# Kernel tuning notes

Hardware: AMD Instinct MI355X
Metric: run time of the kernel (lower is better)

The kernel has to match this reference:

```python
import jax, jax.numpy as jnp
import numpy as np

N = 50000      # points
K = 16         # neighbors per point
DIM = 256      # channels
H = 8          # heads
HD = DIM // H  # head dim


def setup_inputs() -> dict:
    key = jax.random.key(0)
    ks = jax.random.split(key, 8)
    feats = jax.random.normal(ks[0], (N, DIM), jnp.float32)
    xyz = jax.random.normal(ks[1], (N, 3), jnp.float32)
    # sorted segment ids: each point attends to exactly K neighbors
    index_0 = jnp.repeat(jnp.arange(N, dtype=jnp.int32), K)            # [M]
    index_1 = jax.random.randint(ks[2], (N * K,), 0, N, dtype=jnp.int32)  # [M]
    index_0_offsets = jnp.arange(N + 1, dtype=jnp.int32) * K
    s = 1.0 / np.sqrt(DIM)
    qkv_w = jax.random.normal(ks[3], (3 * DIM, DIM), jnp.float32) * s
    qkv_b = jax.random.normal(ks[4], (3 * DIM,), jnp.float32) * 0.01
    proj_w = jax.random.normal(ks[5], (DIM, DIM), jnp.float32) * s
    proj_b = jax.random.normal(ks[6], (DIM,), jnp.float32) * 0.01
    return {
        'feats': feats, 'xyz': xyz,
        'index_0': index_0, 'index_1': index_1,
        'index_0_offsets': index_0_offsets, 'n_max': K,
        'qkv_w': qkv_w, 'qkv_b': qkv_b, 'proj_w': proj_w, 'proj_b': proj_b,
    }


def reference(feats, xyz, index_0, index_1, index_0_offsets, n_max,
              qkv_w, qkv_b, proj_w, proj_b):
    n, c = feats.shape
    scale = (c // H) ** (-0.5)
    qkv = (feats @ qkv_w.T + qkv_b).reshape(n, 3, H, HD)  # [N,3,H,HD]
    q = qkv[:, 0] * scale
    k = qkv[:, 1]
    v = qkv[:, 2]
    # attention_step1: per-pair gathered dot product -> [M, H]
    attn = jnp.einsum('mhd,mhd->mh', q[index_0], k[index_1])
    # scatter_softmax over segments of index_0 (numerically stable)
    seg_max = jax.ops.segment_max(attn, index_0, num_segments=n)  # [N,H]
    e = jnp.exp(attn - seg_max[index_0])
    denom = jax.ops.segment_sum(e, index_0, num_segments=n)       # [N,H]
    attn = e / denom[index_0]                                     # [M,H]
    # attention_step2: scatter weighted sum of gathered values -> [N,H,HD]
    x = jax.ops.segment_sum(attn[:, :, None] * v[index_1], index_0,
                            num_segments=n)
    x = x.reshape(n, c)
    return x @ proj_w.T + proj_b
```

## Files before the change

kernel.cpp:

```cpp
#include <hip/hip_runtime.h>
#include <hip/hip_bf16.h>
#include <stdint.h>

typedef __bf16 bf16x8_t __attribute__((ext_vector_type(8)));
typedef float f32x4_t __attribute__((ext_vector_type(4)));

__device__ __forceinline__ float b2f(unsigned short u) {
    union { uint32_t i; float f; } x; x.i = ((uint32_t)u) << 16; return x.f;
}
__device__ __forceinline__ unsigned short f2b(float f) {
    union { float f; uint32_t i; } x; x.f = f;
    uint32_t r = (x.i + 0x7fffu + ((x.i >> 16) & 1u)) >> 16;
    return (unsigned short)r;
}

#define QSCALE 0.17677669529663687f

__global__ void cvt_f32_bf16(const float* __restrict__ in, unsigned short* __restrict__ out, int n) {
    int i = (blockIdx.x * blockDim.x + threadIdx.x) * 4;
    if (i >= n) return;
    const float4 v = *reinterpret_cast<const float4*>(in + i);
    ushort4 o;
    o.x = f2b(v.x); o.y = f2b(v.y); o.z = f2b(v.z); o.w = f2b(v.w);
    *reinterpret_cast<ushort4*>(out + i) = o;
}

__global__ void prep_weights(const float* __restrict__ qkv_w, const float* __restrict__ proj_w,
                             const float* __restrict__ qkv_b,
                             unsigned short* __restrict__ qkvwb, unsigned short* __restrict__ projwb,
                             float* __restrict__ qkvbS) {
    const int idx = blockIdx.x * 256 + threadIdx.x;
    if (idx < 49152) {
        const int e = idx * 4;
        const float4 v = *reinterpret_cast<const float4*>(qkv_w + e);
        const float sc = (e >> 8) < 256 ? QSCALE : 1.f;
        ushort4 o;
        o.x = f2b(v.x * sc); o.y = f2b(v.y * sc); o.z = f2b(v.z * sc); o.w = f2b(v.w * sc);
        *reinterpret_cast<ushort4*>(qkvwb + e) = o;
    } else if (idx < 49152 + 16384) {
        const int e = (idx - 49152) * 4;
        const float4 v = *reinterpret_cast<const float4*>(proj_w + e);
        ushort4 o;
        o.x = f2b(v.x); o.y = f2b(v.y); o.z = f2b(v.z); o.w = f2b(v.w);
        *reinterpret_cast<ushort4*>(projwb + e) = o;
    } else if (idx < 49152 + 16384 + 192) {
        const int e = (idx - 49152 - 16384) * 4;
        float4 v = *reinterpret_cast<const float4*>(qkv_b + e);
        if (e < 256) { v.x *= QSCALE; v.y *= QSCALE; v.z *= QSCALE; v.w *= QSCALE; }
        *reinterpret_cast<float4*>(qkvbS + e) = v;
    }
}

template <int OUT_MODE>
__launch_bounds__(256, 2)
__global__ void gemm_bf16(const unsigned short* __restrict__ A,
                          const unsigned short* __restrict__ W,
                          const float* __restrict__ bias,
                          void* __restrict__ Cout,
                          int M, int Nn, int Kk) {
    const int nCol = Nn >> 7;
    const int p = blockIdx.x;
    const int xcd = p & 7;
    const int q = p >> 3;
    const int c = q % nCol;
    const int rr = q / nCol;
    const int r = rr * 8 + xcd;
    const int blockRow = r * 128;
    if (blockRow >= M) return;
    const int blockCol = c * 128;

    __shared__ unsigned short As[128 * 64];
    __shared__ unsigned short Bs[128 * 64];
    const int t = threadIdx.x;
    const int w = t >> 6;
    const int l = t & 63;
    const int wm = w >> 1, wn = w & 1;

    f32x4_t acc[4][4];
#pragma unroll
    for (int i = 0; i < 4; ++i)
#pragma unroll
        for (int j = 0; j < 4; ++j) acc[i][j] = (f32x4_t)0.f;

    const int srow = t >> 3;
    const int scol = (((t & 7) ^ ((t >> 3) & 7)) * 8);

    for (int k0 = 0; k0 < Kk; k0 += 64) {
#pragma unroll
        for (int cc = 0; cc < 4; ++cc) {
            int arow = blockRow + cc * 32 + srow;
            arow = arow < M ? arow : M - 1;
            const unsigned short* ga = A + (size_t)arow * Kk + k0 + scol;
            const int brow = blockCol + cc * 32 + srow;
            const unsigned short* gb = W + (size_t)brow * Kk + k0 + scol;
            unsigned short* la = &As[cc * 2048 + w * 512];
            unsigned short* lb = &Bs[cc * 2048 + w * 512];
            __builtin_amdgcn_global_load_lds((const __attribute__((address_space(1))) void*)ga,
                                             (__attribute__((address_space(3))) void*)la, 16, 0, 0);
            __builtin_amdgcn_global_load_lds((const __attribute__((address_space(1))) void*)gb,
                                             (__attribute__((address_space(3))) void*)lb, 16, 0, 0);
        }
        __syncthreads();
        const int l15 = l & 15;
        const int lk = l >> 4;
        const int key = l & 7;
#pragma unroll
        for (int kc = 0; kc < 2; ++kc) {
            bf16x8_t af[4], bfr[4];
            const int cb = kc * 4 + lk;
            const int kof = (cb ^ key) * 8;
#pragma unroll
            for (int i = 0; i < 4; ++i) {
                af[i]  = *reinterpret_cast<const bf16x8_t*>(&As[(wm * 64 + i * 16 + l15) * 64 + kof]);
                bfr[i] = *reinterpret_cast<const bf16x8_t*>(&Bs[(wn * 64 + i * 16 + l15) * 64 + kof]);
            }
#pragma unroll
            for (int i = 0; i < 4; ++i)
#pragma unroll
                for (int j = 0; j < 4; ++j)
                    acc[i][j] = __builtin_amdgcn_mfma_f32_16x16x32_bf16(af[i], bfr[j], acc[i][j], 0, 0, 0);
        }
        __syncthreads();
    }

    const int lr = (l >> 4) * 4;
    const int lc = l & 15;
#pragma unroll
    for (int i = 0; i < 4; ++i) {
#pragma unroll
        for (int j = 0; j < 4; ++j) {
            const int col = blockCol + wn * 64 + j * 16 + lc;
            const float bz = bias[col];
#pragma unroll
            for (int rg = 0; rg < 4; ++rg) {
                const int row = blockRow + wm * 64 + i * 16 + lr + rg;
                if (row < M) {
                    const float val = acc[i][j][rg] + bz;
                    if (OUT_MODE == 0) {
                        ((float*)Cout)[(size_t)row * Nn + col] = val;
                    } else {
                        const size_t sec = (size_t)(col >> 8) * (size_t)M * 256;
                        ((unsigned short*)Cout)[sec + (size_t)row * 256 + (col & 255)] = f2b(val);
                    }
                }
            }
        }
    }
}

__global__ void attn_logits(const unsigned short* __restrict__ qb,
                            const unsigned short* __restrict__ kb,
                            const int* __restrict__ index_1,
                            unsigned short* __restrict__ wbuf) {
    const int w = threadIdx.x >> 6;
    const int i = blockIdx.x * 4 + w;
    const int l = threadIdx.x & 63;
    const int h = l >> 3;
    const int p = l & 7;
    const int d0 = p * 4;

    int nbr[16];
#pragma unroll
    for (int m = 0; m < 16; ++m) nbr[m] = index_1[i * 16 + m];

    ushort4 kreg[16];
#pragma unroll
    for (int m = 0; m < 16; ++m)
        kreg[m] = *reinterpret_cast<const ushort4*>(&kb[(size_t)nbr[m] * 256 + h * 32 + d0]);

    const ushort4 qu = *reinterpret_cast<const ushort4*>(&qb[(size_t)i * 256 + h * 32 + d0]);
    const float qx = b2f(qu.x), qy = b2f(qu.y), qz = b2f(qu.z), qw = b2f(qu.w);

    float s[16];
#pragma unroll
    for (int m = 0; m < 16; ++m) {
        float pv = qx * b2f(kreg[m].x) + qy * b2f(kreg[m].y)
                 + qz * b2f(kreg[m].z) + qw * b2f(kreg[m].w);
        pv += __shfl_xor(pv, 1, 8);
        pv += __shfl_xor(pv, 2, 8);
        pv += __shfl_xor(pv, 4, 8);
        s[m] = pv;
    }
    float mx = -1e30f;
#pragma unroll
    for (int m = 0; m < 16; ++m) mx = fmaxf(mx, s[m]);
    float sum = 0.f;
#pragma unroll
    for (int m = 0; m < 16; ++m) { s[m] = __expf(s[m] - mx); sum += s[m]; }
    const float inv = 1.f / sum;

    const uint32_t pack = (uint32_t)f2b(s[2 * p] * inv) | ((uint32_t)f2b(s[2 * p + 1] * inv) << 16);
    ((uint32_t*)wbuf)[(size_t)i * 64 + h * 8 + p] = pack;
}

__global__ void attn_out(const unsigned short* __restrict__ vb,
                         const unsigned short* __restrict__ wbuf,
                         const int* __restrict__ index_1,
                         unsigned short* __restrict__ xb) {
    const int w = threadIdx.x >> 6;
    const int i = blockIdx.x * 4 + w;
    const int l = threadIdx.x & 63;
    const int h = l >> 3;
    const int p = l & 7;
    const int d0 = p * 4;

    int nbr[16];
#pragma unroll
    for (int m = 0; m < 16; ++m) nbr[m] = index_1[i * 16 + m];

    ushort4 vreg[16];
#pragma unroll
    for (int m = 0; m < 16; ++m)
        vreg[m] = *reinterpret_cast<const ushort4*>(&vb[(size_t)nbr[m] * 256 + h * 32 + d0]);

    const uint32_t wp = ((const uint32_t*)wbuf)[(size_t)i * 64 + h * 8 + p];

    float ax = 0.f, ay = 0.f, az = 0.f, aw = 0.f;
#pragma unroll
    for (int m = 0; m < 16; ++m) {
        const uint32_t src = __shfl(wp, h * 8 + (m >> 1), 64);
        const float wt = b2f((unsigned short)((m & 1) ? (src >> 16) : (src & 0xffff)));
        ax += wt * b2f(vreg[m].x); ay += wt * b2f(vreg[m].y);
        az += wt * b2f(vreg[m].z); aw += wt * b2f(vreg[m].w);
    }
    ushort4 o;
    o.x = f2b(ax); o.y = f2b(ay); o.z = f2b(az); o.w = f2b(aw);
    *reinterpret_cast<ushort4*>(&xb[(size_t)i * 256 + h * 32 + d0]) = o;
}

extern "C" void kernel_launch(void* const* d_in, const int* in_sizes, int n_in,
                              void* d_out, int out_size, void* d_ws, size_t ws_size,
                              hipStream_t stream) {
    const float* feats   = (const float*)d_in[0];
    const int*   index_1 = (const int*)d_in[3];
    const float* qkv_w   = (const float*)d_in[6];
    const float* qkv_b   = (const float*)d_in[7];
    const float* proj_w  = (const float*)d_in[8];
    const float* proj_b  = (const float*)d_in[9];
    float* out = (float*)d_out;

    const int N = 50000, DIM = 256, QKVD = 768;

    unsigned short* featsb = (unsigned short*)d_ws;
    unsigned short* qkvwb  = featsb + (size_t)N * DIM;
    unsigned short* projwb = qkvwb + (size_t)QKVD * DIM;
    float*          qkvbS  = (float*)(projwb + (size_t)DIM * DIM);
    unsigned short* qb     = (unsigned short*)(qkvbS + QKVD);
    unsigned short* kb     = qb + (size_t)N * DIM;
    unsigned short* vb     = kb + (size_t)N * DIM;
    unsigned short* xb     = vb + (size_t)N * DIM;
    unsigned short* wbuf   = xb + (size_t)N * DIM;

    cvt_f32_bf16<<<(N * DIM / 4 + 255) / 256, 256, 0, stream>>>(feats, featsb, N * DIM);
    prep_weights<<<(49152 + 16384 + 192 + 255) / 256, 256, 0, stream>>>(
        qkv_w, proj_w, qkv_b, qkvwb, projwb, qkvbS);

    const int nRow = (N + 127) / 128;
    const int nRowPad = ((nRow + 7) / 8) * 8;

    gemm_bf16<1><<<nRowPad * (QKVD / 128), 256, 0, stream>>>(featsb, qkvwb, qkvbS, qb, N, QKVD, DIM);
    attn_logits<<<N / 4, 256, 0, stream>>>(qb, kb, index_1, wbuf);
    attn_out<<<N / 4, 256, 0, stream>>>(vb, wbuf, index_1, xb);
    gemm_bf16<0><<<nRowPad * (DIM / 128), 256, 0, stream>>>(xb, projwb, proj_b, out, N, DIM, DIM);
}
```

Baseline: 294.4 us.

## Remap attention kernels to one thread per point-head and merge prep kernels

The logits and aggregation kernels now give each thread a whole head (32 dims) of one point, with 8 points per wavefront. Each thread issues 16-byte loads and does the dot products serially, which removes the cross-lane shuffle reductions and the weight broadcast shuffles. The weight buffer layout changes to per-head contiguous 16 weights. The feature conversion and weight prep kernels are merged into one launch. The cost is much higher register use per thread (32 accumulators plus 64 bytes per neighbour load), which may lower occupancy, and less coalesced access across lanes.

```diff
diff --git a/kernel.cpp b/kernel.cpp
--- a/kernel.cpp
+++ b/kernel.cpp
@@ -13,38 +13,42 @@
     uint32_t r = (x.i + 0x7fffu + ((x.i >> 16) & 1u)) >> 16;
     return (unsigned short)r;
 }
+__device__ __forceinline__ void up2(uint32_t d, float& lo, float& hi) {
+    union { uint32_t u; float f; } a, b;
+    a.u = d << 16; b.u = d & 0xffff0000u;
+    lo = a.f; hi = b.f;
+}
 
 #define QSCALE 0.17677669529663687f
-
-__global__ void cvt_f32_bf16(const float* __restrict__ in, unsigned short* __restrict__ out, int n) {
-    int i = (blockIdx.x * blockDim.x + threadIdx.x) * 4;
-    if (i >= n) return;
-    const float4 v = *reinterpret_cast<const float4*>(in + i);
-    ushort4 o;
-    o.x = f2b(v.x); o.y = f2b(v.y); o.z = f2b(v.z); o.w = f2b(v.w);
-    *reinterpret_cast<ushort4*>(out + i) = o;
-}
-
-__global__ void prep_weights(const float* __restrict__ qkv_w, const float* __restrict__ proj_w,
-                             const float* __restrict__ qkv_b,
-                             unsigned short* __restrict__ qkvwb, unsigned short* __restrict__ projwb,
-                             float* __restrict__ qkvbS) {
+#define NQ 50000
+
+__global__ void prep_all(const float* __restrict__ feats, const float* __restrict__ qkv_w,
+                         const float* __restrict__ proj_w, const float* __restrict__ qkv_b,
+                         unsigned short* __restrict__ featsb, unsigned short* __restrict__ qkvwb,
+                         unsigned short* __restrict__ projwb, float* __restrict__ qkvbS) {
     const int idx = blockIdx.x * 256 + threadIdx.x;
-    if (idx < 49152) {
+    const int NF = NQ * 256 / 4;
+    if (idx < NF) {
         const int e = idx * 4;
+        const float4 v = *reinterpret_cast<const float4*>(feats + e);
+        ushort4 o;
+        o.x = f2b(v.x); o.y = f2b(v.y); o.z = f2b(v.z); o.w = f2b(v.w);
+        *reinterpret_cast<ushort4*>(featsb + e) = o;
+    } else if (idx < NF + 49152) {
+        const int e = (idx - NF) * 4;
         const float4 v = *reinterpret_cast<const float4*>(qkv_w + e);
         const float sc = (e >> 8) < 256 ? QSCALE : 1.f;
         ushort4 o;
         o.x = f2b(v.x * sc); o.y = f2b(v.y * sc); o.z = f2b(v.z * sc); o.w = f2b(v.w * sc);
         *reinterpret_cast<ushort4*>(qkvwb + e) = o;
-    } else if (idx < 49152 + 16384) {
-        const int e = (idx - 49152) * 4;
+    } else if (idx < NF + 49152 + 16384) {
+        const int e = (idx - NF - 49152) * 4;
         const float4 v = *reinterpret_cast<const float4*>(proj_w + e);
         ushort4 o;
         o.x = f2b(v.x); o.y = f2b(v.y); o.z = f2b(v.z); o.w = f2b(v.w);
         *reinterpret_cast<ushort4*>(projwb + e) = o;
-    } else if (idx < 49152 + 16384 + 192) {
-        const int e = (idx - 49152 - 16384) * 4;
+    } else if (idx < NF + 49152 + 16384 + 192) {
+        const int e = (idx - NF - 49152 - 16384) * 4;
         float4 v = *reinterpret_cast<const float4*>(qkv_b + e);
         if (e < 256) { v.x *= QSCALE; v.y *= QSCALE; v.z *= QSCALE; v.w *= QSCALE; }
         *reinterpret_cast<float4*>(qkvbS + e) = v;
@@ -148,84 +152,118 @@
     }
 }
 
-__global__ void attn_logits(const unsigned short* __restrict__ qb,
-                            const unsigned short* __restrict__ kb,
-                            const int* __restrict__ index_1,
-                            unsigned short* __restrict__ wbuf) {
+__global__ void attn_logits2(const unsigned short* __restrict__ qb,
+                             const unsigned short* __restrict__ kb,
+                             const int* __restrict__ index_1,
+                             unsigned short* __restrict__ wbuf) {
     const int w = threadIdx.x >> 6;
-    const int i = blockIdx.x * 4 + w;
     const int l = threadIdx.x & 63;
-    const int h = l >> 3;
-    const int p = l & 7;
-    const int d0 = p * 4;
-
-    int nbr[16];
-#pragma unroll
-    for (int m = 0; m < 16; ++m) nbr[m] = index_1[i * 16 + m];
-
-    ushort4 kreg[16];
-#pragma unroll
-    for (int m = 0; m < 16; ++m)
-        kreg[m] = *reinterpret_cast<const ushort4*>(&kb[(size_t)nbr[m] * 256 + h * 32 + d0]);
-
-    const ushort4 qu = *reinterpret_cast<const ushort4*>(&qb[(size_t)i * 256 + h * 32 + d0]);
-    const float qx = b2f(qu.x), qy = b2f(qu.y), qz = b2f(qu.z), qw = b2f(qu.w);
+    const int g = l >> 3;
+    const int h = l & 7;
+    int i = blockIdx.x * 32 + w * 8 + g;
+    const bool valid = i < NQ;
+    if (!valid) i = 0;
+
+    const int4* ip = reinterpret_cast<const int4*>(index_1 + (size_t)i * 16);
+    const int4 n0 = ip[0], n1 = ip[1], n2 = ip[2], n3 = ip[3];
+    const int nbr[16] = { n0.x, n0.y, n0.z, n0.w, n1.x, n1.y, n1.z, n1.w,
+                          n2.x, n2.y, n2.z, n2.w, n3.x, n3.y, n3.z, n3.w };
+
+    const uint4* qp = reinterpret_cast<const uint4*>(qb + (size_t)i * 256 + h * 32);
+    const uint4 q0 = qp[0], q1 = qp[1], q2 = qp[2], q3 = qp[3];
+    const uint32_t qd[16] = { q0.x, q0.y, q0.z, q0.w, q1.x, q1.y, q1.z, q1.w,
+                              q2.x, q2.y, q2.z, q2.w, q3.x, q3.y, q3.z, q3.w };
+    float qf[32];
+#pragma unroll
+    for (int j = 0; j < 16; ++j) up2(qd[j], qf[2 * j], qf[2 * j + 1]);
 
     float s[16];
 #pragma unroll
     for (int m = 0; m < 16; ++m) {
-        float pv = qx * b2f(kreg[m].x) + qy * b2f(kreg[m].y)
-                 + qz * b2f(kreg[m].z) + qw * b2f(kreg[m].w);
-        pv += __shfl_xor(pv, 1, 8);
-        pv += __shfl_xor(pv, 2, 8);
-        pv += __shfl_xor(pv, 4, 8);
-        s[m] = pv;
-    }
-    float mx = -1e30f;
-#pragma unroll
-    for (int m = 0; m < 16; ++m) mx = fmaxf(mx, s[m]);
+        const uint4* kp = reinterpret_cast<const uint4*>(kb + (size_t)nbr[m] * 256 + h * 32);
+        const uint4 k0 = kp[0], k1 = kp[1], k2 = kp[2], k3 = kp[3];
+        const uint32_t kd[16] = { k0.x, k0.y, k0.z, k0.w, k1.x, k1.y, k1.z, k1.w,
+                                  k2.x, k2.y, k2.z, k2.w, k3.x, k3.y, k3.z, k3.w };
+        float acc = 0.f;
+#pragma unroll
+        for (int j = 0; j < 16; ++j) {
+            float lo, hi; up2(kd[j], lo, hi);
+            acc += qf[2 * j] * lo;
+            acc += qf[2 * j + 1] * hi;
+        }
+        s[m] = acc;
+    }
+    float mx = s[0];
+#pragma unroll
+    for (int m = 1; m < 16; ++m) mx = fmaxf(mx, s[m]);
     float sum = 0.f;
 #pragma unroll
     for (int m = 0; m < 16; ++m) { s[m] = __expf(s[m] - mx); sum += s[m]; }
     const float inv = 1.f / sum;
 
-    const uint32_t pack = (uint32_t)f2b(s[2 * p] * inv) | ((uint32_t)f2b(s[2 * p + 1] * inv) << 16);
-    ((uint32_t*)wbuf)[(size_t)i * 64 + h * 8 + p] = pack;
-}
-
-__global__ void attn_out(const unsigned short* __restrict__ vb,
-                         const unsigned short* __restrict__ wbuf,
-                         const int* __restrict__ index_1,
-                         unsigned short* __restrict__ xb) {
+    if (valid) {
+        uint32_t o[8];
+#pragma unroll
+        for (int m = 0; m < 8; ++m)
+            o[m] = (uint32_t)f2b(s[2 * m] * inv) | ((uint32_t)f2b(s[2 * m + 1] * inv) << 16);
+        uint4* op = reinterpret_cast<uint4*>(wbuf + (size_t)i * 128 + h * 16);
+        op[0] = make_uint4(o[0], o[1], o[2], o[3]);
+        op[1] = make_uint4(o[4], o[5], o[6], o[7]);
+    }
+}
+
+__global__ void attn_out2(const unsigned short* __restrict__ vb,
+                          const unsigned short* __restrict__ wbuf,
+                          const int* __restrict__ index_1,
+                          unsigned short* __restrict__ xb) {
     const int w = threadIdx.x >> 6;
-    const int i = blockIdx.x * 4 + w;
     const int l = threadIdx.x & 63;
-    const int h = l >> 3;
-    const int p = l & 7;
-    const int d0 = p * 4;
-
-    int nbr[16];
-#pragma unroll
-    for (int m = 0; m < 16; ++m) nbr[m] = index_1[i * 16 + m];
-
-    ushort4 vreg[16];
-#pragma unroll
-    for (int m = 0; m < 16; ++m)
-        vreg[m] = *reinterpret_cast<const ushort4*>(&vb[(size_t)nbr[m] * 256 + h * 32 + d0]);
-
-    const uint32_t wp = ((const uint32_t*)wbuf)[(size_t)i * 64 + h * 8 + p];
-
-    float ax = 0.f, ay = 0.f, az = 0.f, aw = 0.f;
+    const int g = l >> 3;
+    const int h = l & 7;
+    int i = blockIdx.x * 32 + w * 8 + g;
+    const bool valid = i < NQ;
+    if (!valid) i = 0;
+
+    const int4* ip = reinterpret_cast<const int4*>(index_1 + (size_t)i * 16);
+    const int4 n0 = ip[0], n1 = ip[1], n2 = ip[2], n3 = ip[3];
+    const int nbr[16] = { n0.x, n0.y, n0.z, n0.w, n1.x, n1.y, n1.z, n1.w,
+                          n2.x, n2.y, n2.z, n2.w, n3.x, n3.y, n3.z, n3.w };
+
+    const uint4* wp = reinterpret_cast<const uint4*>(wbuf + (size_t)i * 128 + h * 16);
+    const uint4 w0 = wp[0], w1 = wp[1];
+    const uint32_t wd[8] = { w0.x, w0.y, w0.z, w0.w, w1.x, w1.y, w1.z, w1.w };
+    float wt[16];
+#pragma unroll
+    for (int j = 0; j < 8; ++j) up2(wd[j], wt[2 * j], wt[2 * j + 1]);
+
+    float acc[32];
+#pragma unroll
+    for (int j = 0; j < 32; ++j) acc[j] = 0.f;
+
 #pragma unroll
     for (int m = 0; m < 16; ++m) {
-        const uint32_t src = __shfl(wp, h * 8 + (m >> 1), 64);
-        const float wt = b2f((unsigned short)((m & 1) ? (src >> 16) : (src & 0xffff)));
-        ax += wt * b2f(vreg[m].x); ay += wt * b2f(vreg[m].y);
-        az += wt * b2f(vreg[m].z); aw += wt * b2f(vreg[m].w);
-    }
-    ushort4 o;
-    o.x = f2b(ax); o.y = f2b(ay); o.z = f2b(az); o.w = f2b(aw);
-    *reinterpret_cast<ushort4*>(&xb[(size_t)i * 256 + h * 32 + d0]) = o;
+        const uint4* vp = reinterpret_cast<const uint4*>(vb + (size_t)nbr[m] * 256 + h * 32);
+        const uint4 v0 = vp[0], v1 = vp[1], v2 = vp[2], v3 = vp[3];
+        const uint32_t vd[16] = { v0.x, v0.y, v0.z, v0.w, v1.x, v1.y, v1.z, v1.w,
+                                  v2.x, v2.y, v2.z, v2.w, v3.x, v3.y, v3.z, v3.w };
+#pragma unroll
+        for (int j = 0; j < 16; ++j) {
+            float lo, hi; up2(vd[j], lo, hi);
+            acc[2 * j]     += wt[m] * lo;
+            acc[2 * j + 1] += wt[m] * hi;
+        }
+    }
+    if (valid) {
+        uint32_t o[16];
+#pragma unroll
+        for (int j = 0; j < 16; ++j)
+            o[j] = (uint32_t)f2b(acc[2 * j]) | ((uint32_t)f2b(acc[2 * j + 1]) << 16);
+        uint4* op = reinterpret_cast<uint4*>(xb + (size_t)i * 256 + h * 32);
+        op[0] = make_uint4(o[0], o[1], o[2], o[3]);
+        op[1] = make_uint4(o[4], o[5], o[6], o[7]);
+        op[2] = make_uint4(o[8], o[9], o[10], o[11]);
+        op[3] = make_uint4(o[12], o[13], o[14], o[15]);
+    }
 }
 
 extern "C" void kernel_launch(void* const* d_in, const int* in_sizes, int n_in,
@@ -239,7 +277,7 @@
     const float* proj_b  = (const float*)d_in[9];
     float* out = (float*)d_out;
 
-    const int N = 50000, DIM = 256, QKVD = 768;
+    const int N = NQ, DIM = 256, QKVD = 768;
 
     unsigned short* featsb = (unsigned short*)d_ws;
     unsigned short* qkvwb  = featsb + (size_t)N * DIM;
@@ -251,15 +289,15 @@
     unsigned short* xb     = vb + (size_t)N * DIM;
     unsigned short* wbuf   = xb + (size_t)N * DIM;
 
-    cvt_f32_bf16<<<(N * DIM / 4 + 255) / 256, 256, 0, stream>>>(feats, featsb, N * DIM);
-    prep_weights<<<(49152 + 16384 + 192 + 255) / 256, 256, 0, stream>>>(
-        qkv_w, proj_w, qkv_b, qkvwb, projwb, qkvbS);
+    const int prepQuads = N * 256 / 4 + 49152 + 16384 + 192;
+    prep_all<<<(prepQuads + 255) / 256, 256, 0, stream>>>(
+        feats, qkv_w, proj_w, qkv_b, featsb, qkvwb, projwb, qkvbS);
 
     const int nRow = (N + 127) / 128;
     const int nRowPad = ((nRow + 7) / 8) * 8;
 
     gemm_bf16<1><<<nRowPad * (QKVD / 128), 256, 0, stream>>>(featsb, qkvwb, qkvbS, qb, N, QKVD, DIM);
-    attn_logits<<<N / 4, 256, 0, stream>>>(qb, kb, index_1, wbuf);
-    attn_out<<<N / 4, 256, 0, stream>>>(vb, wbuf, index_1, xb);
+    attn_logits2<<<(N + 31) / 32, 256, 0, stream>>>(qb, kb, index_1, wbuf);
+    attn_out2<<<(N + 31) / 32, 256, 0, stream>>>(vb, wbuf, index_1, xb);
     gemm_bf16<0><<<nRowPad * (DIM / 128), 256, 0, stream>>>(xb, projwb, proj_b, out, N, DIM, DIM);
 }
```

New measurement: 430.3 us. +46.2%, slower.
